# Kernel tuning notes

Measured on AMD Instinct MI355X. Metric: run time of the kernel, lower is better.

Reference implementation:

```python
import jax, jax.numpy as jnp
import numpy as np

N, F, H, R, B, L, C, E, NB = 8192, 512, 256, 16, 32, 256, 7, 262144, 30
D = F + H


def setup_inputs() -> dict:
    ks = jax.random.split(jax.random.key(0), 16)
    g = lambda k, shape, fan: jax.random.normal(k, shape, jnp.float32) / np.sqrt(fan)
    return {
        "x": jax.random.normal(ks[0], (N, F), jnp.float32),
        "edge_index": jax.random.randint(ks[1], (2, E), 0, N),
        "edge_norm": jax.random.uniform(ks[2], (E,), jnp.float32),
        "edge_type": jax.random.randint(ks[3], (E,), 0, R),
        "seq_lengths": jnp.full((B,), L, dtype=jnp.int32),
        "umask": jnp.ones((B, L), jnp.float32),
        "nodal_attn": 1,
        "avec": 0,
        "basis": g(ks[4], (NB, F, H), F),
        "comp": g(ks[5], (R, NB), NB),
        "root1": g(ks[6], (F, H), F),
        "bias1": jnp.zeros((H,), jnp.float32),
        "w_rel": g(ks[7], (H, H), H),
        "b_rel": jnp.zeros((H,), jnp.float32),
        "w_root": g(ks[8], (H, H), H),
        "w_att": g(ks[9], (D, D), D),
        "b_att": jnp.zeros((D,), jnp.float32),
        "w_lin": g(ks[10], (D, H), D),
        "b_lin": jnp.zeros((H,), jnp.float32),
        "w_fc": g(ks[11], (H, C), H),
        "b_fc": jnp.zeros((C,), jnp.float32),
    }


def reference(x, edge_index, edge_norm, edge_type, seq_lengths, umask,
              nodal_attn, avec, basis, comp, root1, bias1, w_rel, b_rel,
              w_root, w_att, b_att, w_lin, b_lin, w_fc, b_fc):
    n = x.shape[0]
    r = comp.shape[0]
    src, dst = edge_index[0], edge_index[1]
    # ---- RGCNConv (num_bases basis decomposition, mean aggregation per relation, root + bias)
    W = jnp.einsum('rb,bfh->rfh', comp, basis)             # [R,F,H]
    xw = jnp.einsum('nf,rfh->nrh', x, W)                   # [N,R,H]
    msg = xw[src, edge_type]                               # [E,H] gather per edge
    seg = dst * r + edge_type                              # per (node, relation) segment
    cnt = jax.ops.segment_sum(jnp.ones((msg.shape[0],), msg.dtype), seg, num_segments=n * r)
    msg = msg / jnp.maximum(cnt[seg], 1.0)[:, None]
    out1 = jax.ops.segment_sum(msg, dst, num_segments=n) + x @ root1 + bias1
    # ---- GraphConv (add aggregation): W_rel * sum_j h_j + b_rel + W_root * h_i
    agg2 = jax.ops.segment_sum(out1[src], dst, num_segments=n)
    out2 = agg2 @ w_rel + b_rel + out1 @ w_root
    emotions = jnp.concatenate([x, out2], axis=-1)          # [N, F+H]
    if int(nodal_attn):
        seq = np.asarray(seq_lengths)                       # static conversation lengths
        starts = np.concatenate([[0], np.cumsum(seq)[:-1]])
        lmax = int(seq.max())
        rows = [jnp.pad(jax.lax.dynamic_slice_in_dim(emotions, int(s), int(l)),
                        ((0, lmax - int(l)), (0, 0)))
                for s, l in zip(starts, seq)]
        M = jnp.stack(rows, 0).transpose(1, 0, 2)           # [L, B, D]
        mask = umask                                        # [B, L]
        # MatchingAttention 'general2', vectorized over all timesteps t
        X = M @ w_att + b_att                               # transform(x_t) for every t: [L,B,D]
        Mm = M * mask.T[:, :, None]                         # mask memory over seq dim
        scores = jnp.einsum('tbd,sbd->tbs', X, Mm) * mask[None]
        a = jax.nn.softmax(jnp.tanh(scores), axis=-1) * mask[None]
        a = a / jnp.sum(a, axis=-1, keepdims=True)
        att = jnp.einsum('tbs,sbd->tbd', a, M)              # [L,B,D]
        hidden = jax.nn.relu(att @ w_lin + b_lin)
    else:
        hidden = jax.nn.relu(emotions @ w_lin + b_lin)
    # dropout is identity in eval mode
    logits = hidden @ w_fc + b_fc
    if int(avec):
        return logits
    return jax.nn.log_softmax(logits, axis=1)  # faithful: torch uses dim=1
```

## Files before the change

### kernel.cpp

```cpp
#include <hip/hip_runtime.h>
#include <hip/hip_bf16.h>

#define NN 8192
#define FF 512
#define HH 256
#define RR 16
#define BB 32
#define LL 256
#define CC 7
#define EE 262144
#define NBASE 30
#define DD 768

constexpr int FLAG_BIAS = 1, FLAG_ACC = 2, FLAG_RELU = 4, FLAG_TANH = 8,
              FLAG_SPLITOUT = 16, FLAG_TAILOUT = 32;

typedef __attribute__((ext_vector_type(8))) short bf16x8;
typedef __attribute__((ext_vector_type(4))) float f32x4;

__global__ __launch_bounds__(256) void detect_dtype(const unsigned short* __restrict__ xs,
                                                    int* __restrict__ flag) {
  __shared__ int red[256];
  int cnt = 0;
  for (int i = threadIdx.x * 2; i < 8192; i += 512) {
    unsigned short u = xs[i];
    int e = (u >> 7) & 0xFF;
    if (e >= 0xC0) cnt++;
  }
  red[threadIdx.x] = cnt;
  __syncthreads();
  for (int s = 128; s > 0; s >>= 1) {
    if (threadIdx.x < s) red[threadIdx.x] += red[threadIdx.x + s];
    __syncthreads();
  }
  if (threadIdx.x == 0) flag[0] = (red[0] > 16) ? 1 : 0;
}

struct ConvSeg {
  const void* src;
  float* dst;
  __hip_bfloat16* hi;
  __hip_bfloat16* lo;
  int n;
  int zero;
};
struct ConvTable {
  ConvSeg seg[12];
  int count;
  long total;
};

__global__ __launch_bounds__(256) void conv_all(ConvTable t, const int* __restrict__ flag) {
  const int fp32 = flag[0];
  for (long i = (long)blockIdx.x * 256 + threadIdx.x; i < t.total;
       i += (long)gridDim.x * 256) {
    long off = i;
    int s = 0;
    while (off >= t.seg[s].n) { off -= t.seg[s].n; s++; }
    const ConvSeg& sg = t.seg[s];
    float v = 0.f;
    if (!sg.zero)
      v = fp32 ? ((const float*)sg.src)[off]
               : __bfloat162float(((const __hip_bfloat16*)sg.src)[off]);
    if (sg.dst) sg.dst[off] = v;
    if (sg.hi) {
      __hip_bfloat16 h = __float2bfloat16(v);
      sg.hi[off] = h;
      sg.lo[off] = __float2bfloat16(v - __bfloat162float(h));
    }
  }
}

__global__ __launch_bounds__(256) void split_t_b16(const void* __restrict__ src,
                                                   __hip_bfloat16* __restrict__ hi,
                                                   __hip_bfloat16* __restrict__ lo,
                                                   int R, int C, const int* __restrict__ flag) {
  const int fp32 = flag[0];
  int total = R * C;
  for (int idx = blockIdx.x * 256 + threadIdx.x; idx < total; idx += gridDim.x * 256) {
    int r = idx % R, c = idx / R;
    float v = fp32 ? ((const float*)src)[(long)r * C + c]
                   : __bfloat162float(((const __hip_bfloat16*)src)[(long)r * C + c]);
    __hip_bfloat16 h = __float2bfloat16(v);
    hi[idx] = h;
    lo[idx] = __float2bfloat16(v - __bfloat162float(h));
  }
}

__global__ __launch_bounds__(256) void split_f32(const float* __restrict__ src,
                                                 __hip_bfloat16* __restrict__ hi,
                                                 __hip_bfloat16* __restrict__ lo, int n) {
  for (int i = blockIdx.x * 256 + threadIdx.x; i < n; i += gridDim.x * 256) {
    float v = src[i];
    __hip_bfloat16 h = __float2bfloat16(v);
    hi[i] = h;
    lo[i] = __float2bfloat16(v - __bfloat162float(h));
  }
}

__global__ __launch_bounds__(256) void transpose_b16(
    const __hip_bfloat16* __restrict__ src, __hip_bfloat16* __restrict__ dst) {
  __shared__ __hip_bfloat16 t[32][33];
  const long b = blockIdx.z;
  const int d0 = blockIdx.x * 32, s0 = blockIdx.y * 32;
  const int c = threadIdx.x & 31, rw = threadIdx.x >> 5;
  const __hip_bfloat16* sp = src + b * (LL * DD);
  __hip_bfloat16* dp = dst + b * (LL * DD);
#pragma unroll
  for (int i = 0; i < 4; ++i)
    t[rw + i * 8][c] = sp[(long)(s0 + rw + i * 8) * DD + d0 + c];
  __syncthreads();
#pragma unroll
  for (int i = 0; i < 4; ++i)
    dp[(long)(d0 + rw + i * 8) * LL + s0 + c] = t[c][rw + i * 8];
}

__global__ __launch_bounds__(256) void wt_gemm(
    const float* __restrict__ basis, const float* __restrict__ comp,
    float* __restrict__ wt_nat) {
  __shared__ float cs[RR * NBASE];
  int tid = threadIdx.x;
  for (int i = tid; i < RR * NBASE; i += 256) cs[i] = comp[i];
  __syncthreads();
  long col = (long)blockIdx.x * 256 + tid;
  float acc[RR] = {};
  for (int b = 0; b < NBASE; ++b) {
    float v = basis[(long)b * 131072 + col];
#pragma unroll
    for (int r = 0; r < RR; ++r) acc[r] += cs[r * NBASE + b] * v;
  }
#pragma unroll
  for (int r = 0; r < RR; ++r) wt_nat[(long)r * 131072 + col] = acc[r];
}

__global__ __launch_bounds__(256) void wt_transpose(
    const float* __restrict__ wt_nat,
    __hip_bfloat16* __restrict__ hi, __hip_bfloat16* __restrict__ lo) {
  __shared__ float t[32][33];
  const int r = blockIdx.z;
  const int f0 = blockIdx.y * 32, h0 = blockIdx.x * 32;
  const int c = threadIdx.x & 31, rw = threadIdx.x >> 5;
  const float* src = wt_nat + ((long)r * 512 + f0) * 256 + h0;
#pragma unroll
  for (int i = 0; i < 4; ++i)
    t[rw + i * 8][c] = src[(long)(rw + i * 8) * 256 + c];
  __syncthreads();
#pragma unroll
  for (int i = 0; i < 4; ++i) {
    int hh = rw + i * 8;
    float v = t[c][hh];
    long orow = (long)(r * 256 + h0 + hh) * 512 + f0 + c;
    __hip_bfloat16 hv = __float2bfloat16(v);
    hi[orow] = hv;
    lo[orow] = __float2bfloat16(v - __bfloat162float(hv));
  }
}

__device__ __forceinline__ void gload_lds16(const void* g, void* l) {
  __builtin_amdgcn_global_load_lds(
      (const __attribute__((address_space(1))) unsigned int*)g,
      (__attribute__((address_space(3))) unsigned int*)l, 16, 0, 0);
}

__global__ __launch_bounds__(256) void mfma_dual(
    const __hip_bfloat16* __restrict__ A, const __hip_bfloat16* __restrict__ Alo,
    const __hip_bfloat16* __restrict__ Bt, const __hip_bfloat16* __restrict__ Btlo,
    const float* __restrict__ bias, float* __restrict__ C, float* __restrict__ Ct,
    __hip_bfloat16* __restrict__ Chi, __hip_bfloat16* __restrict__ Clo,
    int K, int ldc, long sA, long sB, long sC, int flags) {
  __shared__ __hip_bfloat16 Ah[128 * 32];
  __shared__ __hip_bfloat16 Bh[128 * 32];
  __shared__ __hip_bfloat16 Al[128 * 32];
  __shared__ __hip_bfloat16 Bl[128 * 32];
  const int tid = threadIdx.x;
  const int w = tid >> 6, lane = tid & 63;
  const long z = blockIdx.z;
  const long row0 = (long)blockIdx.y * 128, col0 = (long)blockIdx.x * 128;
  const int wm = w & 1, wn = w >> 1;
  const int srow0 = (w * 128 + lane) >> 2;
  const int srow1 = (w * 128 + 64 + lane) >> 2;
  const int kch = (lane & 3) * 8;
  const int fr = lane & 15, q = lane >> 4;
  const bool hasAlo = (Alo != nullptr);
  const __hip_bfloat16* Az = A + z * sA;
  const __hip_bfloat16* Alz = hasAlo ? (Alo + z * sA) : nullptr;
  const __hip_bfloat16* Bz = Bt + z * sB;
  const __hip_bfloat16* Blz = Btlo + z * sB;
  const long aoff0 = (row0 + srow0) * K + kch, aoff1 = (row0 + srow1) * K + kch;
  const long boff0 = (col0 + srow0) * K + kch, boff1 = (col0 + srow1) * K + kch;
  f32x4 acc[4][4] = {};
  for (int k0 = 0; k0 < K; k0 += 32) {
    gload_lds16(Az + aoff0 + k0, Ah + w * 1024);
    gload_lds16(Az + aoff1 + k0, Ah + w * 1024 + 512);
    gload_lds16(Bz + boff0 + k0, Bh + w * 1024);
    gload_lds16(Bz + boff1 + k0, Bh + w * 1024 + 512);
    gload_lds16(Blz + boff0 + k0, Bl + w * 1024);
    gload_lds16(Blz + boff1 + k0, Bl + w * 1024 + 512);
    if (hasAlo) {
      gload_lds16(Alz + aoff0 + k0, Al + w * 1024);
      gload_lds16(Alz + aoff1 + k0, Al + w * 1024 + 512);
    }
    __syncthreads();
    bf16x8 ah[4], bh[4], bl[4];
#pragma unroll
    for (int i = 0; i < 4; ++i) {
      ah[i] = *(const bf16x8*)&Ah[(wm * 64 + i * 16 + fr) * 32 + q * 8];
      bh[i] = *(const bf16x8*)&Bh[(wn * 64 + i * 16 + fr) * 32 + q * 8];
      bl[i] = *(const bf16x8*)&Bl[(wn * 64 + i * 16 + fr) * 32 + q * 8];
    }
#pragma unroll
    for (int i = 0; i < 4; ++i)
#pragma unroll
      for (int j = 0; j < 4; ++j) {
        acc[i][j] = __builtin_amdgcn_mfma_f32_16x16x32_bf16(ah[i], bh[j], acc[i][j], 0, 0, 0);
        acc[i][j] = __builtin_amdgcn_mfma_f32_16x16x32_bf16(ah[i], bl[j], acc[i][j], 0, 0, 0);
      }
    if (hasAlo) {
      bf16x8 al[4];
#pragma unroll
      for (int i = 0; i < 4; ++i)
        al[i] = *(const bf16x8*)&Al[(wm * 64 + i * 16 + fr) * 32 + q * 8];
#pragma unroll
      for (int i = 0; i < 4; ++i)
#pragma unroll
        for (int j = 0; j < 4; ++j)
          acc[i][j] = __builtin_amdgcn_mfma_f32_16x16x32_bf16(al[i], bh[j], acc[i][j], 0, 0, 0);
    }
    __syncthreads();
  }
  const int cr = (lane >> 4) * 4, cc = lane & 15;
  float* Cz = C ? (C + z * sC) : nullptr;
  __hip_bfloat16* Chz = Chi ? (Chi + z * sC) : nullptr;
  __hip_bfloat16* Clz = Clo ? (Clo + z * sC) : nullptr;
#pragma unroll
  for (int i = 0; i < 4; ++i) {
    long rbase = row0 + wm * 64 + i * 16 + cr;
#pragma unroll
    for (int j = 0; j < 4; ++j) {
      long col = col0 + wn * 64 + j * 16 + cc;
      float bv = (flags & FLAG_BIAS) ? bias[col] : 0.f;
#pragma unroll
      for (int r = 0; r < 4; ++r) {
        float v = acc[i][j][r] + bv;
        if (flags & FLAG_RELU) v = fmaxf(v, 0.f);
        if (flags & FLAG_TANH) v = tanhf(v);
        if (flags & FLAG_SPLITOUT) {
          long off = (rbase + r) * ldc + col;
          __hip_bfloat16 hv = __float2bfloat16(v);
          Chz[off] = hv;
          Clz[off] = __float2bfloat16(v - __bfloat162float(hv));
        } else if ((flags & FLAG_TAILOUT) && col >= 4096) {
          Ct[(rbase + r) * 256 + (col - 4096)] = v;
        } else {
          Cz[(rbase + r) * ldc + col] = v;
        }
      }
    }
  }
}

__global__ __launch_bounds__(256) void gemm_nn(
    const float* __restrict__ A, const float* __restrict__ B,
    const float* __restrict__ bias, float* __restrict__ C,
    int M, int N, int K, int lda, int ldb, int ldc,
    long sA, long sB, long sC, int flags) {
  const int bz = blockIdx.z;
  A += (long)bz * sA; B += (long)bz * sB; C += (long)bz * sC;
  __shared__ float As[16][68];
  __shared__ float Bs[16][68];
  const int tid = threadIdx.x;
  const int tx = tid & 15, ty = tid >> 4;
  const int row0 = blockIdx.y * 64, col0 = blockIdx.x * 64;
  const int am = tid >> 2, ak = (tid & 3) * 4;
  const int bk = tid >> 4, bn = (tid & 15) * 4;
  float acc[4][4] = {};
  for (int k0 = 0; k0 < K; k0 += 16) {
    const float* Ap = A + (long)(row0 + am) * lda + k0 + ak;
#pragma unroll
    for (int j = 0; j < 4; ++j) As[ak + j][am] = Ap[j];
    const float* Bp = B + (long)(k0 + bk) * ldb + col0 + bn;
#pragma unroll
    for (int j = 0; j < 4; ++j) Bs[bk][bn + j] = Bp[j];
    __syncthreads();
#pragma unroll
    for (int kk = 0; kk < 16; ++kk) {
      float4 av = *(const float4*)&As[kk][ty * 4];
      float4 bv = *(const float4*)&Bs[kk][tx * 4];
      float a[4] = {av.x, av.y, av.z, av.w};
      float b[4] = {bv.x, bv.y, bv.z, bv.w};
#pragma unroll
      for (int i = 0; i < 4; ++i)
#pragma unroll
        for (int j = 0; j < 4; ++j) acc[i][j] += a[i] * b[j];
    }
    __syncthreads();
  }
#pragma unroll
  for (int i = 0; i < 4; ++i) {
    int r = row0 + ty * 4 + i;
#pragma unroll
    for (int j = 0; j < 4; ++j) {
      int c = col0 + tx * 4 + j;
      float v = acc[i][j];
      if (flags & FLAG_BIAS) v += bias[c];
      float* p = C + (long)r * ldc + c;
      if (flags & FLAG_ACC) v += *p;
      if (flags & FLAG_RELU) v = fmaxf(v, 0.f);
      *p = v;
    }
  }
}

__global__ __launch_bounds__(256) void count_edges(
    const int* __restrict__ ei, const int* __restrict__ et, float* __restrict__ cnt) {
  int e = blockIdx.x * 256 + threadIdx.x;
  if (e < EE) atomicAdd(&cnt[ei[EE + e] * RR + et[e]], 1.0f);
}

__global__ __launch_bounds__(256) void scan_rowptr(
    const float* __restrict__ cntf, int* __restrict__ rowptr, int* __restrict__ fill) {
  __shared__ int part[256];
  int tid = threadIdx.x;
  int base = tid * 32;
  int local[32];
  int s = 0;
  for (int i = 0; i < 32; ++i) {
    local[i] = s;
    const float* c = &cntf[(base + i) * RR];
    int d = 0;
#pragma unroll
    for (int r = 0; r < RR; ++r) d += (int)c[r];
    s += d;
  }
  part[tid] = s;
  __syncthreads();
  for (int off = 1; off < 256; off <<= 1) {
    int v = (tid >= off) ? part[tid - off] : 0;
    __syncthreads();
    part[tid] += v;
    __syncthreads();
  }
  int prev = (tid == 0) ? 0 : part[tid - 1];
  for (int i = 0; i < 32; ++i) rowptr[base + i] = prev + local[i];
  if (tid == 255) rowptr[8192] = part[255];
  for (int i = tid; i < 8192; i += 256) fill[i] = 0;
}

__global__ __launch_bounds__(256) void edge_fill(
    const int* __restrict__ ei, const int* __restrict__ et,
    const int* __restrict__ rowptr, int* __restrict__ fill, int* __restrict__ eidx) {
  int e = blockIdx.x * 256 + threadIdx.x;
  if (e < EE) {
    int dst = ei[EE + e];
    int pos = rowptr[dst] + atomicAdd(&fill[dst], 1);
    eidx[pos] = ei[e] | (et[e] << 16);
  }
}

__global__ __launch_bounds__(256) void rgcn_gather(
    const int* __restrict__ rowptr, const int* __restrict__ eidx,
    const float* __restrict__ cntf, const float* __restrict__ xw,
    float* __restrict__ out1) {
  const int dst = blockIdx.x;
  const int h = threadIdx.x;
  __shared__ float inv[RR];
  __shared__ int se[256];
  if (h < RR) inv[h] = 1.0f / fmaxf(cntf[dst * RR + h], 1.0f);
  const int beg = rowptr[dst], end = rowptr[dst + 1];
  float acc = 0.f;
  for (int c0 = beg; c0 < end; c0 += 256) {
    int n = min(256, end - c0);
    __syncthreads();
    if (h < n) se[h] = eidx[c0 + h];
    __syncthreads();
    for (int i = 0; i < n; ++i) {
      int pk = se[i];
      int src = pk & 0xFFFF, r = pk >> 16;
      acc += xw[((long)src << 12) + (r << 8) + h] * inv[r];
    }
  }
  out1[((long)dst << 8) + h] += acc;
}

__global__ __launch_bounds__(256) void graphconv_gather(
    const int* __restrict__ rowptr, const int* __restrict__ eidx,
    const float* __restrict__ out1, float* __restrict__ agg2) {
  const int dst = blockIdx.x;
  const int h = threadIdx.x;
  __shared__ int se[256];
  const int beg = rowptr[dst], end = rowptr[dst + 1];
  float acc = 0.f;
  for (int c0 = beg; c0 < end; c0 += 256) {
    int n = min(256, end - c0);
    __syncthreads();
    if (h < n) se[h] = eidx[c0 + h];
    __syncthreads();
    for (int i = 0; i < n; ++i)
      acc += out1[((long)(se[i] & 0xFFFF) << 8) + h];
  }
  agg2[((long)dst << 8) + h] = acc;
}

__global__ __launch_bounds__(256) void copy_x(
    const float* __restrict__ x, float* __restrict__ em) {
  int idx = blockIdx.x * 256 + threadIdx.x;
  int n = idx >> 9, f = idx & 511;
  em[(long)n * DD + f] = x[idx];
}

__global__ __launch_bounds__(256) void softmax256(const float* __restrict__ S,
                                                  __hip_bfloat16* __restrict__ Ab) {
  __shared__ float red[256];
  long row = blockIdx.x;
  const float* p = S + row * 256;
  int t = threadIdx.x;
  float v = p[t];
  red[t] = v;
  __syncthreads();
  for (int s = 128; s > 0; s >>= 1) {
    if (t < s) red[t] = fmaxf(red[t], red[t + s]);
    __syncthreads();
  }
  float m = red[0];
  __syncthreads();
  float e = __expf(v - m);
  red[t] = e;
  __syncthreads();
  for (int s = 128; s > 0; s >>= 1) {
    if (t < s) red[t] += red[t + s];
    __syncthreads();
  }
  Ab[row * 256 + t] = __float2bfloat16(e / red[0]);
}

__global__ __launch_bounds__(256) void logits_lsm(
    const float* __restrict__ hidden, const float* __restrict__ w_fc,
    const float* __restrict__ b_fc, void* __restrict__ out_v,
    const int* __restrict__ flag) {
  __shared__ float wf[256 * 7];
  __shared__ float lg[224];
  __shared__ float corr[7];
  int t = blockIdx.x;
  int tid = threadIdx.x;
  for (int i = tid; i < 256 * 7; i += 256) wf[i] = w_fc[i];
  __syncthreads();
  if (tid < 224) {
    int b = tid / 7, c = tid % 7;
    const float* hr = hidden + ((long)((b << 8) + t) << 8);
    float s = b_fc[c];
    for (int k = 0; k < 256; ++k) s += hr[k] * wf[k * 7 + c];
    lg[tid] = s;
  }
  __syncthreads();
  if (tid < 7) {
    float m = -1e30f;
    for (int b = 0; b < BB; ++b) m = fmaxf(m, lg[b * 7 + tid]);
    float sum = 0.f;
    for (int b = 0; b < BB; ++b) sum += __expf(lg[b * 7 + tid] - m);
    corr[tid] = m + logf(sum);
  }
  __syncthreads();
  if (tid < 224) {
    float v = lg[tid] - corr[tid % 7];
    if (flag[0]) ((float*)out_v)[t * 224 + tid] = v;
    else ((__hip_bfloat16*)out_v)[t * 224 + tid] = __float2bfloat16(v);
  }
}

extern "C" void kernel_launch(void* const* d_in, const int* in_sizes, int n_in,
                              void* d_out, int out_size, void* d_ws, size_t ws_size,
                              hipStream_t stream) {
  const int* ei = (const int*)d_in[1];
  const int* et = (const int*)d_in[3];

  float* ws = (float*)d_ws;
  int* flag = (int*)d_ws;
  float* p = ws + 16;
  auto alloc = [&](long nf) { float* r = p; p += nf; return r; };
  float* w_rel_f = alloc(65536);
  float* w_root_f = alloc(65536);
  float* w_fc_f = alloc(1792);
  float* b_rel_f = alloc(256);
  float* biasx = alloc(4352);
  float* b_att_f = alloc(768);
  float* b_lin_f = alloc(256);
  float* b_fc_f = alloc(16);
  __hip_bfloat16* wlin_hi = (__hip_bfloat16*)alloc(98304);
  __hip_bfloat16* wlin_lo = (__hip_bfloat16*)alloc(98304);
  float* x_f = alloc(4194304);
  __hip_bfloat16* x_hi = (__hip_bfloat16*)alloc(2097152);
  __hip_bfloat16* x_lo = (__hip_bfloat16*)alloc(2097152);
  __hip_bfloat16* watt_hi = (__hip_bfloat16*)alloc(294912);
  __hip_bfloat16* watt_lo = (__hip_bfloat16*)alloc(294912);
  __hip_bfloat16* wtc_hi = (__hip_bfloat16*)alloc(1114112);
  __hip_bfloat16* wtc_lo = (__hip_bfloat16*)alloc(1114112);
  float* basis_f = alloc(3932160);
  float* comp_f = alloc(512);
  float* xw = alloc(33554432);
  float* cnt = alloc(131072);
  float* out1 = alloc(2097152);
  float* agg2 = alloc(2097152);
  float* hidden = alloc(2097152);
  int* rowptr = (int*)alloc(8208);
  int* fillc = (int*)alloc(8192);
  int* eidx = (int*)alloc(262144);
  float* wt_nat = xw;
  float* em = xw;
  __hip_bfloat16* em_hi = (__hip_bfloat16*)(em + 6291456);
  __hip_bfloat16* em_lo = (__hip_bfloat16*)(em + 9437184);
  __hip_bfloat16* X_hi = (__hip_bfloat16*)(em + 12582912);
  __hip_bfloat16* X_lo = (__hip_bfloat16*)(em + 15728640);
  float* scores = em + 18874368;
  __hip_bfloat16* a_b16 = (__hip_bfloat16*)(em + 20971520);
  __hip_bfloat16* att_hi = (__hip_bfloat16*)(em + 22020096);
  __hip_bfloat16* att_lo = (__hip_bfloat16*)(em + 25165824);
  __hip_bfloat16* emT_hi = (__hip_bfloat16*)em;
  __hip_bfloat16* emT_lo = (__hip_bfloat16*)(em + 3145728);

  detect_dtype<<<1, 256, 0, stream>>>((const unsigned short*)d_in[0], flag);
  ConvTable T{};
  long tot = 0;
  int ns = 0;
  auto seg = [&](const void* s, float* d, __hip_bfloat16* hi, __hip_bfloat16* lo,
                 int n, int z) {
    T.seg[ns].src = s; T.seg[ns].dst = d; T.seg[ns].hi = hi; T.seg[ns].lo = lo;
    T.seg[ns].n = n; T.seg[ns].zero = z; ns++; tot += n;
  };
  seg(d_in[0], x_f, x_hi, x_lo, NN * FF, 0);
  seg(d_in[8], basis_f, nullptr, nullptr, NBASE * FF * HH, 0);
  seg(d_in[9], comp_f, nullptr, nullptr, RR * NBASE, 0);
  seg(d_in[12], w_rel_f, nullptr, nullptr, HH * HH, 0);
  seg(d_in[13], b_rel_f, nullptr, nullptr, HH, 0);
  seg(d_in[14], w_root_f, nullptr, nullptr, HH * HH, 0);
  seg(d_in[16], b_att_f, nullptr, nullptr, DD, 0);
  seg(d_in[18], b_lin_f, nullptr, nullptr, HH, 0);
  seg(d_in[19], w_fc_f, nullptr, nullptr, HH * CC, 0);
  seg(d_in[20], b_fc_f, nullptr, nullptr, CC, 0);
  seg(nullptr, biasx, nullptr, nullptr, 4096, 1);
  seg(d_in[11], biasx + 4096, nullptr, nullptr, HH, 0);
  T.count = ns;
  T.total = tot;
  conv_all<<<4096, 256, 0, stream>>>(T, flag);
  split_t_b16<<<2048, 256, 0, stream>>>(d_in[15], watt_hi, watt_lo, DD, DD, flag);
  split_t_b16<<<768, 256, 0, stream>>>(d_in[17], wlin_hi, wlin_lo, DD, HH, flag);
  split_t_b16<<<512, 256, 0, stream>>>(d_in[10], wtc_hi + 4096 * 512,
                                       wtc_lo + 4096 * 512, FF, HH, flag);

  wt_gemm<<<131072 / 256, 256, 0, stream>>>(basis_f, comp_f, wt_nat);
  wt_transpose<<<dim3(8, 16, 16), 256, 0, stream>>>(wt_nat, wtc_hi, wtc_lo);
  mfma_dual<<<dim3(34, 64, 1), 256, 0, stream>>>(
      x_hi, x_lo, wtc_hi, wtc_lo, biasx, xw, out1, nullptr, nullptr, FF, 4096,
      0, 0, 0, FLAG_BIAS | FLAG_TAILOUT);
  hipMemsetAsync(cnt, 0, 131072 * sizeof(float), stream);
  count_edges<<<EE / 256, 256, 0, stream>>>(ei, et, cnt);
  scan_rowptr<<<1, 256, 0, stream>>>(cnt, rowptr, fillc);
  edge_fill<<<EE / 256, 256, 0, stream>>>(ei, et, rowptr, fillc, eidx);
  rgcn_gather<<<NN, 256, 0, stream>>>(rowptr, eidx, cnt, xw, out1);
  graphconv_gather<<<NN, 256, 0, stream>>>(rowptr, eidx, out1, agg2);
  copy_x<<<(NN * FF) / 256, 256, 0, stream>>>(x_f, em);
  gemm_nn<<<dim3(HH / 64, NN / 64, 1), 256, 0, stream>>>(
      agg2, w_rel_f, b_rel_f, em + FF, NN, HH, HH, HH, HH, DD, 0, 0, 0, FLAG_BIAS);
  gemm_nn<<<dim3(HH / 64, NN / 64, 1), 256, 0, stream>>>(
      out1, w_root_f, nullptr, em + FF, NN, HH, HH, HH, HH, DD, 0, 0, 0, FLAG_ACC);
  split_f32<<<2048, 256, 0, stream>>>(em, em_hi, em_lo, NN * DD);
  transpose_b16<<<dim3(24, 8, 32), 256, 0, stream>>>(em_hi, emT_hi);
  transpose_b16<<<dim3(24, 8, 32), 256, 0, stream>>>(em_lo, emT_lo);
  mfma_dual<<<dim3(6, 64, 1), 256, 0, stream>>>(
      em_hi, em_lo, watt_hi, watt_lo, b_att_f, nullptr, nullptr, X_hi, X_lo, DD, DD,
      0, 0, 0, FLAG_BIAS | FLAG_SPLITOUT);
  mfma_dual<<<dim3(2, 2, BB), 256, 0, stream>>>(
      X_hi, X_lo, em_hi, em_lo, nullptr, scores, nullptr, nullptr, nullptr, DD, LL,
      (long)LL * DD, (long)LL * DD, (long)LL * LL, FLAG_TANH);
  softmax256<<<BB * LL, 256, 0, stream>>>(scores, a_b16);
  mfma_dual<<<dim3(6, 2, BB), 256, 0, stream>>>(
      a_b16, nullptr, emT_hi, emT_lo, nullptr, nullptr, nullptr, att_hi, att_lo, LL, DD,
      (long)LL * LL, (long)LL * DD, (long)LL * DD, FLAG_SPLITOUT);
  mfma_dual<<<dim3(2, 64, 1), 256, 0, stream>>>(
      att_hi, att_lo, wlin_hi, wlin_lo, b_lin_f, hidden, nullptr, nullptr, nullptr,
      DD, HH, 0, 0, 0, FLAG_BIAS | FLAG_RELU);
  logits_lsm<<<LL, 256, 0, stream>>>(hidden, w_fc_f, b_fc_f, d_out, flag);
}
```

Before: 721.4 us.

## Fuse GraphConv rel/root GEMMs into one split-bf16 MFMA and remodel block order

Replaces the two fp32 SIMT gemm_nn calls (W_rel on agg2, W_root on out1) with a single split-bf16 MFMA GEMM over a concatenated [agg2|out1] K=512 operand and stacked transposed weights. The gather kernels now write their results directly as hi/lo bf16 into that concatenated buffer, and x is copied into the embedding buffer already split, so the fp32 em buffer and the split_f32 pass go away. mfma_dual also gains grouped (8-row super-tile) block ordering for better L2 reuse. The costs are extra bf16 hi/lo writes in the gathers and a slight precision change from the split-bf16 arithmetic.

```diff
diff --git a/kernel.cpp b/kernel.cpp
--- a/kernel.cpp
+++ b/kernel.cpp
@@ -12,7 +12,7 @@
 #define NBASE 30
 #define DD 768
 
-constexpr int FLAG_BIAS = 1, FLAG_ACC = 2, FLAG_RELU = 4, FLAG_TANH = 8,
+constexpr int FLAG_BIAS = 1, FLAG_RELU = 4, FLAG_TANH = 8,
               FLAG_SPLITOUT = 16, FLAG_TAILOUT = 32;
 
 typedef __attribute__((ext_vector_type(8))) short bf16x8;
@@ -74,7 +74,8 @@
 __global__ __launch_bounds__(256) void split_t_b16(const void* __restrict__ src,
                                                    __hip_bfloat16* __restrict__ hi,
                                                    __hip_bfloat16* __restrict__ lo,
-                                                   int R, int C, const int* __restrict__ flag) {
+                                                   int R, int C, int ld, int off,
+                                                   const int* __restrict__ flag) {
   const int fp32 = flag[0];
   int total = R * C;
   for (int idx = blockIdx.x * 256 + threadIdx.x; idx < total; idx += gridDim.x * 256) {
@@ -82,20 +83,20 @@
     float v = fp32 ? ((const float*)src)[(long)r * C + c]
                    : __bfloat162float(((const __hip_bfloat16*)src)[(long)r * C + c]);
     __hip_bfloat16 h = __float2bfloat16(v);
-    hi[idx] = h;
-    lo[idx] = __float2bfloat16(v - __bfloat162float(h));
-  }
-}
-
-__global__ __launch_bounds__(256) void split_f32(const float* __restrict__ src,
-                                                 __hip_bfloat16* __restrict__ hi,
-                                                 __hip_bfloat16* __restrict__ lo, int n) {
-  for (int i = blockIdx.x * 256 + threadIdx.x; i < n; i += gridDim.x * 256) {
-    float v = src[i];
-    __hip_bfloat16 h = __float2bfloat16(v);
-    hi[i] = h;
-    lo[i] = __float2bfloat16(v - __bfloat162float(h));
-  }
+    long d = (long)c * ld + off + r;
+    hi[d] = h;
+    lo[d] = __float2bfloat16(v - __bfloat162float(h));
+  }
+}
+
+__global__ __launch_bounds__(256) void copy_xsplit(
+    const __hip_bfloat16* __restrict__ xh, const __hip_bfloat16* __restrict__ xl,
+    __hip_bfloat16* __restrict__ eh, __hip_bfloat16* __restrict__ el) {
+  int idx = blockIdx.x * 256 + threadIdx.x;
+  int n = idx >> 9, f = idx & 511;
+  long d = (long)n * DD + f;
+  eh[d] = xh[idx];
+  el[d] = xl[idx];
 }
 
 __global__ __launch_bounds__(256) void transpose_b16(
@@ -175,7 +176,17 @@
   const int tid = threadIdx.x;
   const int w = tid >> 6, lane = tid & 63;
   const long z = blockIdx.z;
-  const long row0 = (long)blockIdx.y * 128, col0 = (long)blockIdx.x * 128;
+  {
+  }
+  const int nbx = gridDim.x, nby = gridDim.y;
+  const int pid = blockIdx.y * nbx + blockIdx.x;
+  const int G = 8 * nbx;
+  const int gid = pid / G;
+  const int first = gid * 8;
+  const int rows = min(nby - first, 8);
+  const int by = first + (pid % G) % rows;
+  const int bx = (pid % G) / rows;
+  const long row0 = (long)by * 128, col0 = (long)bx * 128;
   const int wm = w & 1, wn = w >> 1;
   const int srow0 = (w * 128 + lane) >> 2;
   const int srow1 = (w * 128 + 64 + lane) >> 2;
@@ -259,58 +270,6 @@
   }
 }
 
-__global__ __launch_bounds__(256) void gemm_nn(
-    const float* __restrict__ A, const float* __restrict__ B,
-    const float* __restrict__ bias, float* __restrict__ C,
-    int M, int N, int K, int lda, int ldb, int ldc,
-    long sA, long sB, long sC, int flags) {
-  const int bz = blockIdx.z;
-  A += (long)bz * sA; B += (long)bz * sB; C += (long)bz * sC;
-  __shared__ float As[16][68];
-  __shared__ float Bs[16][68];
-  const int tid = threadIdx.x;
-  const int tx = tid & 15, ty = tid >> 4;
-  const int row0 = blockIdx.y * 64, col0 = blockIdx.x * 64;
-  const int am = tid >> 2, ak = (tid & 3) * 4;
-  const int bk = tid >> 4, bn = (tid & 15) * 4;
-  float acc[4][4] = {};
-  for (int k0 = 0; k0 < K; k0 += 16) {
-    const float* Ap = A + (long)(row0 + am) * lda + k0 + ak;
-#pragma unroll
-    for (int j = 0; j < 4; ++j) As[ak + j][am] = Ap[j];
-    const float* Bp = B + (long)(k0 + bk) * ldb + col0 + bn;
-#pragma unroll
-    for (int j = 0; j < 4; ++j) Bs[bk][bn + j] = Bp[j];
-    __syncthreads();
-#pragma unroll
-    for (int kk = 0; kk < 16; ++kk) {
-      float4 av = *(const float4*)&As[kk][ty * 4];
-      float4 bv = *(const float4*)&Bs[kk][tx * 4];
-      float a[4] = {av.x, av.y, av.z, av.w};
-      float b[4] = {bv.x, bv.y, bv.z, bv.w};
-#pragma unroll
-      for (int i = 0; i < 4; ++i)
-#pragma unroll
-        for (int j = 0; j < 4; ++j) acc[i][j] += a[i] * b[j];
-    }
-    __syncthreads();
-  }
-#pragma unroll
-  for (int i = 0; i < 4; ++i) {
-    int r = row0 + ty * 4 + i;
-#pragma unroll
-    for (int j = 0; j < 4; ++j) {
-      int c = col0 + tx * 4 + j;
-      float v = acc[i][j];
-      if (flags & FLAG_BIAS) v += bias[c];
-      float* p = C + (long)r * ldc + c;
-      if (flags & FLAG_ACC) v += *p;
-      if (flags & FLAG_RELU) v = fmaxf(v, 0.f);
-      *p = v;
-    }
-  }
-}
-
 __global__ __launch_bounds__(256) void count_edges(
     const int* __restrict__ ei, const int* __restrict__ et, float* __restrict__ cnt) {
   int e = blockIdx.x * 256 + threadIdx.x;
@@ -360,7 +319,8 @@
 __global__ __launch_bounds__(256) void rgcn_gather(
     const int* __restrict__ rowptr, const int* __restrict__ eidx,
     const float* __restrict__ cntf, const float* __restrict__ xw,
-    float* __restrict__ out1) {
+    float* __restrict__ out1, __hip_bfloat16* __restrict__ a2o1_hi,
+    __hip_bfloat16* __restrict__ a2o1_lo) {
   const int dst = blockIdx.x;
   const int h = threadIdx.x;
   __shared__ float inv[RR];
@@ -379,12 +339,18 @@
       acc += xw[((long)src << 12) + (r << 8) + h] * inv[r];
     }
   }
-  out1[((long)dst << 8) + h] += acc;
+  float tot = out1[((long)dst << 8) + h] + acc;
+  out1[((long)dst << 8) + h] = tot;
+  __hip_bfloat16 hv = __float2bfloat16(tot);
+  long d = (long)dst * 512 + 256 + h;
+  a2o1_hi[d] = hv;
+  a2o1_lo[d] = __float2bfloat16(tot - __bfloat162float(hv));
 }
 
 __global__ __launch_bounds__(256) void graphconv_gather(
     const int* __restrict__ rowptr, const int* __restrict__ eidx,
-    const float* __restrict__ out1, float* __restrict__ agg2) {
+    const float* __restrict__ out1, __hip_bfloat16* __restrict__ a2o1_hi,
+    __hip_bfloat16* __restrict__ a2o1_lo) {
   const int dst = blockIdx.x;
   const int h = threadIdx.x;
   __shared__ int se[256];
@@ -398,14 +364,10 @@
     for (int i = 0; i < n; ++i)
       acc += out1[((long)(se[i] & 0xFFFF) << 8) + h];
   }
-  agg2[((long)dst << 8) + h] = acc;
-}
-
-__global__ __launch_bounds__(256) void copy_x(
-    const float* __restrict__ x, float* __restrict__ em) {
-  int idx = blockIdx.x * 256 + threadIdx.x;
-  int n = idx >> 9, f = idx & 511;
-  em[(long)n * DD + f] = x[idx];
+  __hip_bfloat16 hv = __float2bfloat16(acc);
+  long d = (long)dst * 512 + h;
+  a2o1_hi[d] = hv;
+  a2o1_lo[d] = __float2bfloat16(acc - __bfloat162float(hv));
 }
 
 __global__ __launch_bounds__(256) void softmax256(const float* __restrict__ S,
@@ -477,8 +439,6 @@
   int* flag = (int*)d_ws;
   float* p = ws + 16;
   auto alloc = [&](long nf) { float* r = p; p += nf; return r; };
-  float* w_rel_f = alloc(65536);
-  float* w_root_f = alloc(65536);
   float* w_fc_f = alloc(1792);
   float* b_rel_f = alloc(256);
   float* biasx = alloc(4352);
@@ -487,11 +447,12 @@
   float* b_fc_f = alloc(16);
   __hip_bfloat16* wlin_hi = (__hip_bfloat16*)alloc(98304);
   __hip_bfloat16* wlin_lo = (__hip_bfloat16*)alloc(98304);
-  float* x_f = alloc(4194304);
   __hip_bfloat16* x_hi = (__hip_bfloat16*)alloc(2097152);
   __hip_bfloat16* x_lo = (__hip_bfloat16*)alloc(2097152);
   __hip_bfloat16* watt_hi = (__hip_bfloat16*)alloc(294912);
   __hip_bfloat16* watt_lo = (__hip_bfloat16*)alloc(294912);
+  __hip_bfloat16* wrr_hi = (__hip_bfloat16*)alloc(65536);
+  __hip_bfloat16* wrr_lo = (__hip_bfloat16*)alloc(65536);
   __hip_bfloat16* wtc_hi = (__hip_bfloat16*)alloc(1114112);
   __hip_bfloat16* wtc_lo = (__hip_bfloat16*)alloc(1114112);
   float* basis_f = alloc(3932160);
@@ -499,7 +460,8 @@
   float* xw = alloc(33554432);
   float* cnt = alloc(131072);
   float* out1 = alloc(2097152);
-  float* agg2 = alloc(2097152);
+  __hip_bfloat16* a2o1_hi = (__hip_bfloat16*)alloc(2097152);
+  __hip_bfloat16* a2o1_lo = (__hip_bfloat16*)alloc(2097152);
   float* hidden = alloc(2097152);
   int* rowptr = (int*)alloc(8208);
   int* fillc = (int*)alloc(8192);
@@ -526,12 +488,10 @@
     T.seg[ns].src = s; T.seg[ns].dst = d; T.seg[ns].hi = hi; T.seg[ns].lo = lo;
     T.seg[ns].n = n; T.seg[ns].zero = z; ns++; tot += n;
   };
-  seg(d_in[0], x_f, x_hi, x_lo, NN * FF, 0);
+  seg(d_in[0], nullptr, x_hi, x_lo, NN * FF, 0);
   seg(d_in[8], basis_f, nullptr, nullptr, NBASE * FF * HH, 0);
   seg(d_in[9], comp_f, nullptr, nullptr, RR * NBASE, 0);
-  seg(d_in[12], w_rel_f, nullptr, nullptr, HH * HH, 0);
   seg(d_in[13], b_rel_f, nullptr, nullptr, HH, 0);
-  seg(d_in[14], w_root_f, nullptr, nullptr, HH * HH, 0);
   seg(d_in[16], b_att_f, nullptr, nullptr, DD, 0);
   seg(d_in[18], b_lin_f, nullptr, nullptr, HH, 0);
   seg(d_in[19], w_fc_f, nullptr, nullptr, HH * CC, 0);
@@ -541,10 +501,12 @@
   T.count = ns;
   T.total = tot;
   conv_all<<<4096, 256, 0, stream>>>(T, flag);
-  split_t_b16<<<2048, 256, 0, stream>>>(d_in[15], watt_hi, watt_lo, DD, DD, flag);
-  split_t_b16<<<768, 256, 0, stream>>>(d_in[17], wlin_hi, wlin_lo, DD, HH, flag);
+  split_t_b16<<<2048, 256, 0, stream>>>(d_in[15], watt_hi, watt_lo, DD, DD, DD, 0, flag);
+  split_t_b16<<<768, 256, 0, stream>>>(d_in[17], wlin_hi, wlin_lo, DD, HH, DD, 0, flag);
   split_t_b16<<<512, 256, 0, stream>>>(d_in[10], wtc_hi + 4096 * 512,
-                                       wtc_lo + 4096 * 512, FF, HH, flag);
+                                       wtc_lo + 4096 * 512, FF, HH, FF, 0, flag);
+  split_t_b16<<<256, 256, 0, stream>>>(d_in[12], wrr_hi, wrr_lo, HH, HH, 512, 0, flag);
+  split_t_b16<<<256, 256, 0, stream>>>(d_in[14], wrr_hi, wrr_lo, HH, HH, 512, 256, flag);
 
   wt_gemm<<<131072 / 256, 256, 0, stream>>>(basis_f, comp_f, wt_nat);
   wt_transpose<<<dim3(8, 16, 16), 256, 0, stream>>>(wt_nat, wtc_hi, wtc_lo);
@@ -555,14 +517,12 @@
   count_edges<<<EE / 256, 256, 0, stream>>>(ei, et, cnt);
   scan_rowptr<<<1, 256, 0, stream>>>(cnt, rowptr, fillc);
   edge_fill<<<EE / 256, 256, 0, stream>>>(ei, et, rowptr, fillc, eidx);
-  rgcn_gather<<<NN, 256, 0, stream>>>(rowptr, eidx, cnt, xw, out1);
-  graphconv_gather<<<NN, 256, 0, stream>>>(rowptr, eidx, out1, agg2);
-  copy_x<<<(NN * FF) / 256, 256, 0, stream>>>(x_f, em);
-  gemm_nn<<<dim3(HH / 64, NN / 64, 1), 256, 0, stream>>>(
-      agg2, w_rel_f, b_rel_f, em + FF, NN, HH, HH, HH, HH, DD, 0, 0, 0, FLAG_BIAS);
-  gemm_nn<<<dim3(HH / 64, NN / 64, 1), 256, 0, stream>>>(
-      out1, w_root_f, nullptr, em + FF, NN, HH, HH, HH, HH, DD, 0, 0, 0, FLAG_ACC);
-  split_f32<<<2048, 256, 0, stream>>>(em, em_hi, em_lo, NN * DD);
+  rgcn_gather<<<NN, 256, 0, stream>>>(rowptr, eidx, cnt, xw, out1, a2o1_hi, a2o1_lo);
+  graphconv_gather<<<NN, 256, 0, stream>>>(rowptr, eidx, out1, a2o1_hi, a2o1_lo);
+  copy_xsplit<<<(NN * FF) / 256, 256, 0, stream>>>(x_hi, x_lo, em_hi, em_lo);
+  mfma_dual<<<dim3(2, 64, 1), 256, 0, stream>>>(
+      a2o1_hi, a2o1_lo, wrr_hi, wrr_lo, b_rel_f, nullptr, nullptr,
+      em_hi + 512, em_lo + 512, 512, DD, 0, 0, 0, FLAG_BIAS | FLAG_SPLITOUT);
   transpose_b16<<<dim3(24, 8, 32), 256, 0, stream>>>(em_hi, emT_hi);
   transpose_b16<<<dim3(24, 8, 32), 256, 0, stream>>>(em_lo, emT_lo);
   mfma_dual<<<dim3(6, 64, 1), 256, 0, stream>>>(
```

Result: faster. 697.6 us (-3.3%).
